# Kernel optimization log

Measured on AMD Instinct MI355X. Metric: run time of the kernel, lower is better.

The kernel has to match this reference:

```python
import jax, jax.numpy as jnp
import numpy as np

N = 4096        # nodes
IN_FEATS = 256
N_HIDDEN = 128
N_CLASSES = 32
E = 131072      # edges for the GAE blocks (avg degree 32)
TEMP = 0.2
ALPHA = 1.0
EPS = 1e-6
CHUNK = 64      # row-chunk size for masked max aggregation


def _glorot(key, shape):
    fan = shape[0] + shape[1]
    return jax.random.normal(key, shape, jnp.float32) * jnp.sqrt(2.0 / fan)


def setup_inputs():
    key = jax.random.key(0)
    ks = jax.random.split(key, 20)
    return {
        'adj': jax.random.uniform(ks[0], (N, N), jnp.float32),
        'inputs': jax.random.normal(ks[1], (N, IN_FEATS), jnp.float32),
        'feat_inputs': jax.random.normal(ks[2], (N, IN_FEATS), jnp.float32),
        'u': jax.random.uniform(ks[3], (N, N), jnp.float32),
        'src': jax.random.randint(ks[4], (E,), 0, N, jnp.int32),
        'dst': jax.random.randint(ks[5], (E,), 0, N, jnp.int32),
        # GAE GraphConv params (in->hidden, hidden->hidden)
        'gc0_W': _glorot(ks[6], (IN_FEATS, N_HIDDEN)), 'gc0_b': jnp.zeros((N_HIDDEN,), jnp.float32),
        'gc1_W': _glorot(ks[7], (N_HIDDEN, N_HIDDEN)), 'gc1_b': jnp.zeros((N_HIDDEN,), jnp.float32),
        # GraphSAGE layer 0 (in -> hidden), maxpool aggregator
        'p0_W': _glorot(ks[8], (IN_FEATS, IN_FEATS)), 'p0_b': jnp.zeros((IN_FEATS,), jnp.float32),
        'l0_W': _glorot(ks[9], (IN_FEATS, N_HIDDEN)), 'l0_b': jnp.zeros((N_HIDDEN,), jnp.float32),
        'b0': jnp.zeros((N_HIDDEN,), jnp.float32),
        # GraphSAGE layer 1 (hidden -> hidden)
        'p1_W': _glorot(ks[10], (N_HIDDEN, N_HIDDEN)), 'p1_b': jnp.zeros((N_HIDDEN,), jnp.float32),
        'l1_W': _glorot(ks[11], (N_HIDDEN, N_HIDDEN)), 'l1_b': jnp.zeros((N_HIDDEN,), jnp.float32),
        'b1': jnp.zeros((N_HIDDEN,), jnp.float32),
        # GraphSAGE layer 2 (hidden -> classes)
        'p2_W': _glorot(ks[12], (N_HIDDEN, N_HIDDEN)), 'p2_b': jnp.zeros((N_HIDDEN,), jnp.float32),
        'l2_W': _glorot(ks[13], (N_HIDDEN, N_CLASSES)), 'l2_b': jnp.zeros((N_CLASSES,), jnp.float32),
        'b2': jnp.zeros((N_CLASSES,), jnp.float32),
    }


def _graph_conv(h, W, b, src, dst, out_norm, in_norm):
    # DGL GraphConv, norm='both': D_in^{-1/2} A D_out^{-1/2} X W + b
    h = h @ W
    h = h * out_norm[:, None]
    agg = jax.ops.segment_sum(h[src], dst, num_segments=N)
    return agg * in_norm[:, None] + b


def _masked_max(mask, z):
    # h_new[i] = max_{j: mask[i, j]} z[j]; chunk over destination rows to bound memory
    n, d = z.shape
    m = mask.reshape(n // CHUNK, CHUNK, n)
    def body(carry, mc):
        out = jnp.max(jnp.where(mc[:, :, None], z[None, :, :], -jnp.inf), axis=1)
        return carry, out
    _, outs = jax.lax.scan(body, None, m)
    return outs.reshape(n, d)


def _l2norm(x):
    return x / jnp.maximum(jnp.linalg.norm(x, axis=1, keepdims=True), 1e-12)


def _forward(adj, inputs, feat_inputs, u, src, dst,
             gc0_W, gc0_b, gc1_W, gc1_b,
             p0_W, p0_b, l0_W, l0_b, b0,
             p1_W, p1_b, l1_W, l1_b, b1,
             p2_W, p2_b, l2_W, l2_b, b2):
    ones = jnp.ones((E,), jnp.float32)
    out_norm = jnp.maximum(jax.ops.segment_sum(ones, src, num_segments=N), 1.0) ** -0.5
    in_norm = jnp.maximum(jax.ops.segment_sum(ones, dst, num_segments=N), 1.0) ** -0.5
    # --- GAE encode (dropout inactive at inference) ---
    h = jax.nn.relu(_graph_conv(inputs, gc0_W, gc0_b, src, dst, out_norm, in_norm))
    h = _graph_conv(h, gc1_W, gc1_b, src, dst, out_norm, in_norm)
    # --- GAE decode ---
    ep = jax.nn.sigmoid(h @ h.T)
    # --- interpolate ---
    P = ALPHA * (ep / jnp.max(ep)) + (1.0 - ALPHA) * adj
    # --- RelaxedBernoulli straight-through sampling ---
    Pc = jnp.clip(P, EPS, 1.0 - EPS)
    uc = jnp.clip(u, EPS, 1.0 - EPS)
    logits = jnp.log(Pc) - jnp.log1p(-Pc)
    noise = jnp.log(uc) - jnp.log1p(-uc)        # logistic noise
    soft = jax.nn.sigmoid((logits + noise) / TEMP)
    y = soft + jax.lax.stop_gradient(jnp.round(soft) - soft)
    yt = jnp.triu(y, 1)
    A = yt + yt.T
    # --- normalize_adj: diag=1, L1 row normalize; original detaches here ---
    eye = jnp.eye(N, dtype=bool)
    A = jnp.where(eye, 1.0, A)
    A = A / jnp.maximum(jnp.sum(A, axis=1, keepdims=True), 1e-12)
    A = jax.lax.stop_gradient(A)
    mask = A != 0.0   # symmetric graph structure incl. self-loops
    # --- GraphSAGE with maxpool aggregator (dropout inactive) ---
    h = feat_inputs
    layers = ((p0_W, p0_b, l0_W, l0_b, b0, False),
              (p1_W, p1_b, l1_W, l1_b, b1, False),
              (p2_W, p2_b, l2_W, l2_b, b2, True))
    for pW, pb, lW, lb, bb, last in layers:
        z = jax.nn.relu(h @ pW + pb)
        agg = _masked_max(mask, z)
        h = agg @ lW + lb + bb
        if not last:
            h = _l2norm(jax.nn.relu(h))
    return h


def reference(adj, inputs, feat_inputs, u, src, dst,
              gc0_W, gc0_b, gc1_W, gc1_b,
              p0_W, p0_b, l0_W, l0_b, b0,
              p1_W, p1_b, l1_W, l1_b, b1,
              p2_W, p2_b, l2_W, l2_b, b2):
    return _forward(adj, inputs, feat_inputs, u, src, dst,
                    gc0_W, gc0_b, gc1_W, gc1_b,
                    p0_W, p0_b, l0_W, l0_b, b0,
                    p1_W, p1_b, l1_W, l1_b, b1,
                    p2_W, p2_b, l2_W, l2_b, b2)
```

## Files before the change

### kernel.cpp

```cpp
#include <hip/hip_runtime.h>
#include <hip/hip_fp16.h>
#include <cstdint>
#include <cstddef>

#define NN 4096
#define EE 131072
#define TS 64

__device__ __forceinline__ unsigned fkey(float f) {
    unsigned u = __float_as_uint(f);
    return (u & 0x80000000u) ? ~u : (u | 0x80000000u);
}
__device__ __forceinline__ float funkey(unsigned k) {
    unsigned u = (k & 0x80000000u) ? (k & 0x7fffffffu) : ~k;
    return __uint_as_float(u);
}

__device__ __forceinline__ void pkmax(unsigned& a, unsigned x) {
    asm("v_pk_max_f16 %0, %0, %1" : "+v"(a) : "v"(x));
}
__device__ __forceinline__ unsigned bit_sext_s(unsigned w, int off) {
    return (unsigned)(((int)(w << (31 - off))) >> 31);
}

__global__ void k_count(const int* __restrict__ src, const int* __restrict__ dst,
                        int* __restrict__ cs, int* __restrict__ cd) {
    int e = blockIdx.x * 256 + threadIdx.x;
    if (e < EE) {
        atomicAdd(&cs[src[e]], 1);
        atomicAdd(&cd[dst[e]], 1);
    }
}

__global__ void k_norm(const int* __restrict__ cs, const int* __restrict__ cd,
                       float* __restrict__ on, float* __restrict__ inn) {
    int i = blockIdx.x * 256 + threadIdx.x;
    if (i < NN) {
        int a = cs[i] > 1 ? cs[i] : 1;
        int b = cd[i] > 1 ? cd[i] : 1;
        on[i]  = 1.0f / sqrtf((float)a);
        inn[i] = 1.0f / sqrtf((float)b);
    }
}

template<int K, int ND, int RB>
__global__ void k_gemm_scale(const float* __restrict__ X, const float* __restrict__ W,
                             const float* __restrict__ scale, float* __restrict__ out) {
    __shared__ float xr[RB][K];
    int i0 = blockIdx.x * RB;
    for (int t = threadIdx.x; t < RB * K; t += ND)
        xr[t / K][t % K] = X[(size_t)(i0 + t / K) * K + t % K];
    __syncthreads();
    int j = threadIdx.x;
    float acc[RB];
    #pragma unroll
    for (int r = 0; r < RB; ++r) acc[r] = 0.0f;
    #pragma unroll 4
    for (int k = 0; k < K; ++k) {
        float w = W[k * ND + j];
        #pragma unroll
        for (int r = 0; r < RB; ++r) acc[r] = fmaf(xr[r][k], w, acc[r]);
    }
    #pragma unroll
    for (int r = 0; r < RB; ++r)
        out[(size_t)(i0 + r) * ND + j] = acc[r] * scale[i0 + r];
}

template<int K, int ND, int NS, int RB, int L2N, int H16>
__global__ void k_gemm_mrg(const float* __restrict__ X, size_t xstride,
                           const float* __restrict__ W,
                           const float* __restrict__ b1, const float* __restrict__ b2,
                           float* __restrict__ out, int do_relu) {
    __shared__ float xr[RB][K];
    int i0 = blockIdx.x * RB;
    for (int t = threadIdx.x; t < RB * K; t += ND) {
        size_t off = (size_t)(i0 + t / K) * K + t % K;
        float v = X[off];
        #pragma unroll
        for (int s = 1; s < NS; ++s) v = fmaxf(v, X[(size_t)s * xstride + off]);
        xr[t / K][t % K] = v;
    }
    __syncthreads();
    int j = threadIdx.x;
    float acc[RB];
    #pragma unroll
    for (int r = 0; r < RB; ++r) acc[r] = 0.0f;
    #pragma unroll 4
    for (int k = 0; k < K; ++k) {
        float w = W[k * ND + j];
        #pragma unroll
        for (int r = 0; r < RB; ++r) acc[r] = fmaf(xr[r][k], w, acc[r]);
    }
    if constexpr (L2N) {
        float v[RB], ss[RB];
        #pragma unroll
        for (int r = 0; r < RB; ++r) {
            float t = acc[r] + b1[j];
            if (b2) t += b2[j];
            v[r] = fmaxf(t, 0.0f);
            ss[r] = v[r] * v[r];
        }
        #pragma unroll
        for (int o = 1; o < 64; o <<= 1)
            #pragma unroll
            for (int r = 0; r < RB; ++r) ss[r] += __shfl_xor(ss[r], o, 64);
        __shared__ float sred[RB][2];
        if ((threadIdx.x & 63) == 0)
            #pragma unroll
            for (int r = 0; r < RB; ++r) sred[r][threadIdx.x >> 6] = ss[r];
        __syncthreads();
        #pragma unroll
        for (int r = 0; r < RB; ++r) {
            float tot = sred[r][0] + sred[r][1];
            out[(size_t)(i0 + r) * ND + j] = v[r] / fmaxf(sqrtf(tot), 1e-12f);
        }
    } else if constexpr (H16) {
        unsigned* oh = (unsigned*)out;
        #pragma unroll
        for (int r = 0; r < RB; ++r) {
            float v = fmaxf(acc[r] + b1[j], 0.0f);
            float o2 = __shfl_xor(v, 1, 64);
            if ((j & 1) == 0) {
                __half2 h = __floats2half2_rn(v, o2);
                oh[(size_t)(i0 + r) * (ND / 2) + (j >> 1)] = *(unsigned*)&h;
            }
        }
    } else {
        #pragma unroll
        for (int r = 0; r < RB; ++r) {
            float v = acc[r] + b1[j];
            if (b2) v += b2[j];
            if (do_relu) v = fmaxf(v, 0.0f);
            out[(size_t)(i0 + r) * ND + j] = v;
        }
    }
}

__global__ void k_scatter(const float* __restrict__ t, const int* __restrict__ src,
                          const int* __restrict__ dst, float* __restrict__ agg) {
    int e = blockIdx.x;
    int j = threadIdx.x;
    int s = src[e], d = dst[e];
    atomicAdd(&agg[(size_t)d * 128 + j], t[(size_t)s * 128 + j]);
}

__global__ void k_gcn_out(const float* __restrict__ agg, const float* __restrict__ inn,
                          const float* __restrict__ b, float* __restrict__ out, int do_relu) {
    int idx = blockIdx.x * 256 + threadIdx.x;
    int i = idx >> 7, j = idx & 127;
    float v = agg[idx] * inn[i] + b[j];
    if (do_relu) v = fmaxf(v, 0.0f);
    out[idx] = v;
}

template<int MODE>
__global__ __launch_bounds__(256, 4) void k_stile(const float* __restrict__ h,
                                                  const float* __restrict__ u,
                                                  unsigned* __restrict__ smax_key,
                                                  unsigned* __restrict__ mb) {
    int ti = blockIdx.y, tj = blockIdx.x;
    if (tj < ti) return;
    __shared__ float Ah[TS][68];
    __shared__ float Bh[TS][68];
    int tid = threadIdx.x;
    int tx = tid & 15, ty = tid >> 4;
    const float* ha = h + (size_t)ti * TS * 128;
    const float* hb = h + (size_t)tj * TS * 128;

    float acc[4][4];
    #pragma unroll
    for (int r = 0; r < 4; ++r)
        #pragma unroll
        for (int c = 0; c < 4; ++c) acc[r][c] = 0.0f;

    for (int half = 0; half < 2; ++half) {
        __syncthreads();
        #pragma unroll
        for (int t = 0; t < 4; ++t) {
            int f = tid + t * 256;
            int row = f >> 4, kk = f & 15;
            *(float4*)&Ah[row][kk * 4] = *(const float4*)(ha + (size_t)row * 128 + half * 64 + kk * 4);
            *(float4*)&Bh[row][kk * 4] = *(const float4*)(hb + (size_t)row * 128 + half * 64 + kk * 4);
        }
        __syncthreads();
        #pragma unroll 2
        for (int k4 = 0; k4 < 16; ++k4) {
            float4 a[4], b[4];
            #pragma unroll
            for (int r = 0; r < 4; ++r) a[r] = *(const float4*)&Ah[ty + 16 * r][k4 * 4];
            #pragma unroll
            for (int c = 0; c < 4; ++c) b[c] = *(const float4*)&Bh[tx + 16 * c][k4 * 4];
            #pragma unroll
            for (int r = 0; r < 4; ++r)
                #pragma unroll
                for (int c = 0; c < 4; ++c) {
                    acc[r][c] = fmaf(a[r].x, b[c].x, acc[r][c]);
                    acc[r][c] = fmaf(a[r].y, b[c].y, acc[r][c]);
                    acc[r][c] = fmaf(a[r].z, b[c].z, acc[r][c]);
                    acc[r][c] = fmaf(a[r].w, b[c].w, acc[r][c]);
                }
        }
    }

    if constexpr (MODE == 0) {
        float m = -3.4e38f;
        #pragma unroll
        for (int r = 0; r < 4; ++r)
            #pragma unroll
            for (int c = 0; c < 4; ++c) m = fmaxf(m, acc[r][c]);
        #pragma unroll
        for (int o = 1; o < 64; o <<= 1) m = fmaxf(m, __shfl_xor(m, o, 64));
        __shared__ float wm[4];
        if ((tid & 63) == 0) wm[tid >> 6] = m;
        __syncthreads();
        if (tid == 0) {
            float mm = fmaxf(fmaxf(wm[0], wm[1]), fmaxf(wm[2], wm[3]));
            atomicMax(smax_key, fkey(mm));
        }
    } else {
        float smax = funkey(*smax_key);
        float epmax = 1.0f / (1.0f + expf(-smax));
        __shared__ unsigned lm[TS][2];
        __shared__ unsigned lmT[TS][2];
        if (tid < 128) { lm[tid >> 1][tid & 1] = 0u; lmT[tid >> 1][tid & 1] = 0u; }
        __syncthreads();
        #pragma unroll
        for (int r = 0; r < 4; ++r) {
            #pragma unroll
            for (int c = 0; c < 4; ++c) {
                int li = ty + 16 * r, lj = tx + 16 * c;
                int gi = ti * TS + li, gj = tj * TS + lj;
                bool bit = false;
                if (gi < gj) {
                    float ep = 1.0f / (1.0f + expf(-acc[r][c]));
                    float P = ep / epmax;
                    float Pc = fminf(fmaxf(P, 1e-6f), 1.0f - 1e-6f);
                    float uu = u[(size_t)gi * NN + gj];
                    float ucv = fminf(fmaxf(uu, 1e-6f), 1.0f - 1e-6f);
                    bit = Pc > (1.0f - ucv);
                } else if (gi == gj) {
                    bit = true;
                }
                if (bit) {
                    atomicOr(&lm[li][lj >> 5], 1u << (lj & 31));
                    atomicOr(&lmT[lj][li >> 5], 1u << (li & 31));
                }
            }
        }
        __syncthreads();
        if (tid < 128) {
            int r = tid >> 1, wq = tid & 1;
            unsigned word = lm[r][wq];
            if (ti == tj) word |= lmT[r][wq];
            mb[(size_t)(ti * TS + r) * 128 + tj * 2 + wq] = word;
        } else if (ti != tj) {
            int r = (tid - 128) >> 1, wq = tid & 1;
            mb[(size_t)(tj * TS + r) * 128 + ti * 2 + wq] = lmT[r][wq];
        }
    }
}

__global__ __launch_bounds__(256, 4) void k_stile_store(const float* __restrict__ h,
                                                        float* __restrict__ S,
                                                        unsigned* __restrict__ smax_key) {
    int ti = blockIdx.y, tj = blockIdx.x;
    if (tj < ti) return;
    __shared__ float Ah[TS][68];
    __shared__ float Bh[TS][68];
    int tid = threadIdx.x;
    int tx = tid & 15, ty = tid >> 4;
    const float* ha = h + (size_t)ti * TS * 128;
    const float* hb = h + (size_t)tj * TS * 128;

    float acc[4][4];
    #pragma unroll
    for (int r = 0; r < 4; ++r)
        #pragma unroll
        for (int c = 0; c < 4; ++c) acc[r][c] = 0.0f;

    for (int half = 0; half < 2; ++half) {
        __syncthreads();
        #pragma unroll
        for (int t = 0; t < 4; ++t) {
            int f = tid + t * 256;
            int row = f >> 4, kk = f & 15;
            *(float4*)&Ah[row][kk * 4] = *(const float4*)(ha + (size_t)row * 128 + half * 64 + kk * 4);
            *(float4*)&Bh[row][kk * 4] = *(const float4*)(hb + (size_t)row * 128 + half * 64 + kk * 4);
        }
        __syncthreads();
        #pragma unroll 2
        for (int k4 = 0; k4 < 16; ++k4) {
            float4 a[4], b[4];
            #pragma unroll
            for (int r = 0; r < 4; ++r) a[r] = *(const float4*)&Ah[ty + 16 * r][k4 * 4];
            #pragma unroll
            for (int c = 0; c < 4; ++c) b[c] = *(const float4*)&Bh[tx + 16 * c][k4 * 4];
            #pragma unroll
            for (int r = 0; r < 4; ++r)
                #pragma unroll
                for (int c = 0; c < 4; ++c) {
                    acc[r][c] = fmaf(a[r].x, b[c].x, acc[r][c]);
                    acc[r][c] = fmaf(a[r].y, b[c].y, acc[r][c]);
                    acc[r][c] = fmaf(a[r].z, b[c].z, acc[r][c]);
                    acc[r][c] = fmaf(a[r].w, b[c].w, acc[r][c]);
                }
        }
    }

    float* sp = S + (size_t)(ti * 64 + tj) * 4096;
    #pragma unroll
    for (int r = 0; r < 4; ++r)
        #pragma unroll
        for (int c = 0; c < 4; ++c)
            sp[(ty + 16 * r) * 64 + tx + 16 * c] = acc[r][c];

    float m = -3.4e38f;
    #pragma unroll
    for (int r = 0; r < 4; ++r)
        #pragma unroll
        for (int c = 0; c < 4; ++c) m = fmaxf(m, acc[r][c]);
    #pragma unroll
    for (int o = 1; o < 64; o <<= 1) m = fmaxf(m, __shfl_xor(m, o, 64));
    __shared__ float wm[4];
    if ((tid & 63) == 0) wm[tid >> 6] = m;
    __syncthreads();
    if (tid == 0)
        atomicMax(smax_key, fkey(fmaxf(fmaxf(wm[0], wm[1]), fmaxf(wm[2], wm[3]))));
}

__global__ __launch_bounds__(256, 4) void k_bitemit(const float* __restrict__ S,
                                                    const float* __restrict__ u,
                                                    const unsigned* __restrict__ smax_key,
                                                    unsigned* __restrict__ mb) {
    int ti = blockIdx.y, tj = blockIdx.x;
    if (tj < ti) return;
    int tid = threadIdx.x;
    int tx = tid & 15, ty = tid >> 4;
    float smax = funkey(*smax_key);
    float epmax = 1.0f / (1.0f + expf(-smax));
    __shared__ unsigned lm[TS][2];
    __shared__ unsigned lmT[TS][2];
    if (tid < 128) { lm[tid >> 1][tid & 1] = 0u; lmT[tid >> 1][tid & 1] = 0u; }
    __syncthreads();
    const float* sp = S + (size_t)(ti * 64 + tj) * 4096;
    #pragma unroll
    for (int r = 0; r < 4; ++r) {
        #pragma unroll
        for (int c = 0; c < 4; ++c) {
            int li = ty + 16 * r, lj = tx + 16 * c;
            int gi = ti * TS + li, gj = tj * TS + lj;
            bool bit = false;
            if (gi < gj) {
                float ep = 1.0f / (1.0f + expf(-sp[li * 64 + lj]));
                float P = ep / epmax;
                float Pc = fminf(fmaxf(P, 1e-6f), 1.0f - 1e-6f);
                float uu = u[(size_t)gi * NN + gj];
                float ucv = fminf(fmaxf(uu, 1e-6f), 1.0f - 1e-6f);
                bit = Pc > (1.0f - ucv);
            } else if (gi == gj) {
                bit = true;
            }
            if (bit) {
                atomicOr(&lm[li][lj >> 5], 1u << (lj & 31));
                atomicOr(&lmT[lj][li >> 5], 1u << (li & 31));
            }
        }
    }
    __syncthreads();
    if (tid < 128) {
        int r = tid >> 1, wq = tid & 1;
        unsigned word = lm[r][wq];
        if (ti == tj) word |= lmT[r][wq];
        mb[(size_t)(ti * TS + r) * 128 + tj * 2 + wq] = word;
    } else if (ti != tj) {
        int r = (tid - 128) >> 1, wq = tid & 1;
        mb[(size_t)(tj * TS + r) * 128 + ti * 2 + wq] = lmT[r][wq];
    }
}

template<int RT, int JS>
__global__ __launch_bounds__(256, 8) void k_mmax256h(const unsigned* __restrict__ mb,
                                                     const unsigned* __restrict__ zh,
                                                     float* __restrict__ part) {
    constexpr int JPS = NN / JS;
    constexpr int WPS = JPS / 32;
    constexpr int RPG = RT / 4;
    constexpr int NRB = NN / RT;
    int rowblk = blockIdx.x % NRB, js = blockIdx.x / NRB;
    int i0 = rowblk * RT;

    __shared__ unsigned msk[RT][WPS + 1];
    {
        int t = threadIdx.x;
        msk[t / WPS][t % WPS] = mb[(size_t)(i0 + t / WPS) * 128 + js * WPS + t % WPS];
    }
    __syncthreads();

    int d = threadIdx.x & 63;
    int g = threadIdx.x >> 6;
    const uint2* zbase = (const uint2*)zh + (size_t)js * JPS * 64 + d;

    uint2 acc[RPG];
    #pragma unroll
    for (int r = 0; r < RPG; ++r) acc[r] = make_uint2(0u, 0u);

    #pragma unroll 1
    for (int wq = 0; wq < WPS; ++wq) {
        unsigned m[RPG];
        #pragma unroll
        for (int r = 0; r < RPG; ++r)
            m[r] = (unsigned)__builtin_amdgcn_readfirstlane((int)msk[g * RPG + r][wq]);
        const uint2* zp = zbase + (size_t)(wq * 32) * 64;
        #pragma unroll 2
        for (int j4 = 0; j4 < 32; j4 += 4) {
            uint2 z0 = zp[0 * 64];
            uint2 z1 = zp[1 * 64];
            uint2 z2 = zp[2 * 64];
            uint2 z3 = zp[3 * 64];
            #pragma unroll
            for (int r = 0; r < RPG; ++r) {
                unsigned s0 = bit_sext_s(m[r], j4 + 0);
                unsigned s1 = bit_sext_s(m[r], j4 + 1);
                unsigned s2 = bit_sext_s(m[r], j4 + 2);
                unsigned s3 = bit_sext_s(m[r], j4 + 3);
                pkmax(acc[r].x, s0 & z0.x); pkmax(acc[r].y, s0 & z0.y);
                pkmax(acc[r].x, s1 & z1.x); pkmax(acc[r].y, s1 & z1.y);
                pkmax(acc[r].x, s2 & z2.x); pkmax(acc[r].y, s2 & z2.y);
                pkmax(acc[r].x, s3 & z3.x); pkmax(acc[r].y, s3 & z3.y);
            }
            zp += 4 * 64;
        }
    }

    float4* po = (float4*)(part + (size_t)js * NN * 256);
    #pragma unroll
    for (int r = 0; r < RPG; ++r) {
        __half2 h0 = *(__half2*)&acc[r].x;
        __half2 h1 = *(__half2*)&acc[r].y;
        float2 f0 = __half22float2(h0);
        float2 f1 = __half22float2(h1);
        po[(size_t)(i0 + g * RPG + r) * 64 + d] = make_float4(f0.x, f0.y, f1.x, f1.y);
    }
}

template<int RT, int JS>
__global__ __launch_bounds__(256, 8) void k_mmax128h(const unsigned* __restrict__ mb,
                                                     const unsigned* __restrict__ zh,
                                                     float* __restrict__ part) {
    constexpr int JPS = NN / JS;
    constexpr int WPS = JPS / 32;
    constexpr int RPG = RT / 4;
    constexpr int NRB = NN / RT;
    int rowblk = blockIdx.x % NRB, js = blockIdx.x / NRB;
    int i0 = rowblk * RT;

    __shared__ unsigned msk[RT][WPS + 1];
    {
        int t = threadIdx.x;
        msk[t / WPS][t % WPS] = mb[(size_t)(i0 + t / WPS) * 128 + js * WPS + t % WPS];
    }
    __syncthreads();

    int lane = threadIdx.x & 63;
    int g = threadIdx.x >> 6;
    unsigned jpar = lane >> 5;
    int d2 = lane & 31;
    const uint2* zbase = (const uint2*)zh + (size_t)js * JPS * 32 + d2;

    uint2 acc[RPG];
    #pragma unroll
    for (int r = 0; r < RPG; ++r) acc[r] = make_uint2(0u, 0u);

    #pragma unroll 1
    for (int wq = 0; wq < WPS; ++wq) {
        unsigned m[RPG];
        #pragma unroll
        for (int r = 0; r < RPG; ++r)
            m[r] = (unsigned)__builtin_amdgcn_readfirstlane((int)msk[g * RPG + r][wq]);
        const uint2* zp = zbase + (size_t)(wq * 32) * 32;
        #pragma unroll 2
        for (int j4 = 0; j4 < 32; j4 += 4) {
            uint2 za = zp[(size_t)jpar * 32];
            uint2 zb = zp[(size_t)(2 + jpar) * 32];
            int oa = j4 + (int)jpar, ob = j4 + 2 + (int)jpar;
            #pragma unroll
            for (int r = 0; r < RPG; ++r) {
                unsigned sa = bit_sext_s(m[r], oa);
                unsigned sb = bit_sext_s(m[r], ob);
                pkmax(acc[r].x, sa & za.x); pkmax(acc[r].y, sa & za.y);
                pkmax(acc[r].x, sb & zb.x); pkmax(acc[r].y, sb & zb.y);
            }
            zp += 4 * 32;
        }
    }

    #pragma unroll
    for (int r = 0; r < RPG; ++r) {
        unsigned ox = __shfl_xor(acc[r].x, 32, 64);
        unsigned oy = __shfl_xor(acc[r].y, 32, 64);
        pkmax(acc[r].x, ox);
        pkmax(acc[r].y, oy);
    }
    if (!jpar) {
        float4* po = (float4*)(part + (size_t)js * NN * 128);
        #pragma unroll
        for (int r = 0; r < RPG; ++r) {
            __half2 h0 = *(__half2*)&acc[r].x;
            __half2 h1 = *(__half2*)&acc[r].y;
            float2 f0 = __half22float2(h0);
            float2 f1 = __half22float2(h1);
            po[(size_t)(i0 + g * RPG + r) * 32 + d2] = make_float4(f0.x, f0.y, f1.x, f1.y);
        }
    }
}

template<int NS>
__global__ void k_gemm_final(const float* __restrict__ X, size_t xstride,
                             const float* __restrict__ W,
                             const float* __restrict__ b1, const float* __restrict__ b2,
                             float* __restrict__ out) {
    __shared__ float xr[4][128];
    int i0 = blockIdx.x * 4;
    for (int t = threadIdx.x; t < 512; t += 128) {
        int r = t >> 7, k = t & 127;
        float v = X[(size_t)(i0 + r) * 128 + k];
        #pragma unroll
        for (int s = 1; s < NS; ++s)
            v = fmaxf(v, X[(size_t)s * xstride + (size_t)(i0 + r) * 128 + k]);
        xr[r][k] = v;
    }
    __syncthreads();
    int il = threadIdx.x >> 5, j = threadIdx.x & 31;
    float acc = 0.0f;
    #pragma unroll 8
    for (int k = 0; k < 128; ++k) acc = fmaf(xr[il][k], W[k * 32 + j], acc);
    out[(size_t)(i0 + il) * 32 + j] = acc + b1[j] + b2[j];
}

extern "C" void kernel_launch(void* const* d_in, const int* in_sizes, int n_in,
                              void* d_out, int out_size, void* d_ws, size_t ws_size,
                              hipStream_t stream) {
    const float* inputs = (const float*)d_in[1];
    const float* feat   = (const float*)d_in[2];
    const float* u      = (const float*)d_in[3];
    const int*   src    = (const int*)d_in[4];
    const int*   dst    = (const int*)d_in[5];
    const float* gc0W = (const float*)d_in[6],  *gc0b = (const float*)d_in[7];
    const float* gc1W = (const float*)d_in[8],  *gc1b = (const float*)d_in[9];
    const float* p0W  = (const float*)d_in[10], *p0b  = (const float*)d_in[11];
    const float* l0W  = (const float*)d_in[12], *l0b  = (const float*)d_in[13];
    const float* b0   = (const float*)d_in[14];
    const float* p1W  = (const float*)d_in[15], *p1b  = (const float*)d_in[16];
    const float* l1W  = (const float*)d_in[17], *l1b  = (const float*)d_in[18];
    const float* b1   = (const float*)d_in[19];
    const float* p2W  = (const float*)d_in[20], *p2b  = (const float*)d_in[21];
    const float* l2W  = (const float*)d_in[22], *l2b  = (const float*)d_in[23];
    const float* b2   = (const float*)d_in[24];
    float* out = (float*)d_out;

    const size_t MB = 1048576;
    char* w = (char*)d_ws;
    int*      cnt_src  = (int*)(w + 0);
    int*      cnt_dst  = (int*)(w + 16384);
    float*    on       = (float*)(w + 32768);
    float*    inn      = (float*)(w + 49152);
    unsigned* smax_key = (unsigned*)(w + 65536);
    char*     big      = w + 131072;
    float*    tmp      = (float*)(big);
    float*    agg      = (float*)(big + 2 * MB);
    float*    hbuf     = (float*)(big + 4 * MB);
    unsigned* mb       = (unsigned*)(big + 6 * MB);
    unsigned* zh       = (unsigned*)(big + 8 * MB);
    float*    pm       = (float*)(big + 12 * MB);
    float*    hs       = (float*)(big + 44 * MB);
    float*    Sbuf     = (float*)(big + 46 * MB);
    bool use_sstore = ws_size >= 131072 + 110 * MB;

    hipMemsetAsync(w, 0, 131072, stream);
    k_count<<<EE / 256, 256, 0, stream>>>(src, dst, cnt_src, cnt_dst);
    k_norm<<<NN / 256, 256, 0, stream>>>(cnt_src, cnt_dst, on, inn);

    k_gemm_scale<256, 128, 4><<<NN / 4, 128, 0, stream>>>(inputs, gc0W, on, tmp);
    hipMemsetAsync(agg, 0, (size_t)NN * 128 * 4, stream);
    k_scatter<<<EE, 128, 0, stream>>>(tmp, src, dst, agg);
    k_gcn_out<<<NN * 128 / 256, 256, 0, stream>>>(agg, inn, gc0b, hbuf, 1);

    k_gemm_scale<128, 128, 4><<<NN / 4, 128, 0, stream>>>(hbuf, gc1W, on, tmp);
    hipMemsetAsync(agg, 0, (size_t)NN * 128 * 4, stream);
    k_scatter<<<EE, 128, 0, stream>>>(tmp, src, dst, agg);
    k_gcn_out<<<NN * 128 / 256, 256, 0, stream>>>(agg, inn, gc1b, hbuf, 0);

    dim3 tg(64, 64);
    if (use_sstore) {
        k_stile_store<<<tg, 256, 0, stream>>>(hbuf, Sbuf, smax_key);
        k_bitemit<<<tg, 256, 0, stream>>>(Sbuf, u, smax_key, mb);
    } else {
        k_stile<0><<<tg, 256, 0, stream>>>(hbuf, nullptr, smax_key, nullptr);
        k_stile<1><<<tg, 256, 0, stream>>>(hbuf, u, smax_key, mb);
    }

    k_gemm_mrg<256, 256, 1, 4, 0, 1><<<NN / 4, 256, 0, stream>>>(feat, 0, p0W, p0b, nullptr, (float*)zh, 1);
    k_mmax256h<16, 8><<<(NN / 16) * 8, 256, 0, stream>>>(mb, zh, pm);
    k_gemm_mrg<256, 128, 8, 4, 1, 0><<<NN / 4, 128, 0, stream>>>(pm, (size_t)NN * 256, l0W, l0b, b0, hs, 0);

    k_gemm_mrg<128, 128, 1, 4, 0, 1><<<NN / 4, 128, 0, stream>>>(hs, 0, p1W, p1b, nullptr, (float*)zh, 1);
    k_mmax128h<16, 8><<<(NN / 16) * 8, 256, 0, stream>>>(mb, zh, pm);
    k_gemm_mrg<128, 128, 8, 4, 1, 0><<<NN / 4, 128, 0, stream>>>(pm, (size_t)NN * 128, l1W, l1b, b1, tmp, 0);

    k_gemm_mrg<128, 128, 1, 4, 0, 1><<<NN / 4, 128, 0, stream>>>(tmp, 0, p2W, p2b, nullptr, (float*)zh, 1);
    k_mmax128h<16, 8><<<(NN / 16) * 8, 256, 0, stream>>>(mb, zh, pm);
    k_gemm_final<8><<<NN / 4, 128, 0, stream>>>(pm, (size_t)NN * 128, l2W, l2b, b2, out);
}
```

Baseline: 673.5 us.

## Store masked-max partials as packed fp16 and batch edges per block in scatter

```diff
diff --git a/kernel.cpp b/kernel.cpp
--- a/kernel.cpp
+++ b/kernel.cpp
@@ -66,20 +66,13 @@
         out[(size_t)(i0 + r) * ND + j] = acc[r] * scale[i0 + r];
 }
 
-template<int K, int ND, int NS, int RB, int L2N, int H16>
-__global__ void k_gemm_mrg(const float* __restrict__ X, size_t xstride,
-                           const float* __restrict__ W,
-                           const float* __restrict__ b1, const float* __restrict__ b2,
-                           float* __restrict__ out, int do_relu) {
+template<int K, int ND, int RB, int H16>
+__global__ void k_gemm_ab(const float* __restrict__ X, const float* __restrict__ W,
+                          const float* __restrict__ b1, float* __restrict__ out) {
     __shared__ float xr[RB][K];
     int i0 = blockIdx.x * RB;
-    for (int t = threadIdx.x; t < RB * K; t += ND) {
-        size_t off = (size_t)(i0 + t / K) * K + t % K;
-        float v = X[off];
-        #pragma unroll
-        for (int s = 1; s < NS; ++s) v = fmaxf(v, X[(size_t)s * xstride + off]);
-        xr[t / K][t % K] = v;
-    }
+    for (int t = threadIdx.x; t < RB * K; t += ND)
+        xr[t / K][t % K] = X[(size_t)(i0 + t / K) * K + t % K];
     __syncthreads();
     int j = threadIdx.x;
     float acc[RB];
@@ -91,30 +84,7 @@
         #pragma unroll
         for (int r = 0; r < RB; ++r) acc[r] = fmaf(xr[r][k], w, acc[r]);
     }
-    if constexpr (L2N) {
-        float v[RB], ss[RB];
-        #pragma unroll
-        for (int r = 0; r < RB; ++r) {
-            float t = acc[r] + b1[j];
-            if (b2) t += b2[j];
-            v[r] = fmaxf(t, 0.0f);
-            ss[r] = v[r] * v[r];
-        }
-        #pragma unroll
-        for (int o = 1; o < 64; o <<= 1)
-            #pragma unroll
-            for (int r = 0; r < RB; ++r) ss[r] += __shfl_xor(ss[r], o, 64);
-        __shared__ float sred[RB][2];
-        if ((threadIdx.x & 63) == 0)
-            #pragma unroll
-            for (int r = 0; r < RB; ++r) sred[r][threadIdx.x >> 6] = ss[r];
-        __syncthreads();
-        #pragma unroll
-        for (int r = 0; r < RB; ++r) {
-            float tot = sred[r][0] + sred[r][1];
-            out[(size_t)(i0 + r) * ND + j] = v[r] / fmaxf(sqrtf(tot), 1e-12f);
-        }
-    } else if constexpr (H16) {
+    if constexpr (H16) {
         unsigned* oh = (unsigned*)out;
         #pragma unroll
         for (int r = 0; r < RB; ++r) {
@@ -127,10 +97,68 @@
         }
     } else {
         #pragma unroll
+        for (int r = 0; r < RB; ++r)
+            out[(size_t)(i0 + r) * ND + j] = acc[r] + b1[j];
+    }
+}
+
+template<int K, int ND, int NS, int RB, int L2N>
+__global__ void k_gemm_mrgh(const unsigned* __restrict__ Xh, size_t xstride,
+                            const float* __restrict__ W,
+                            const float* __restrict__ b1, const float* __restrict__ b2,
+                            float* __restrict__ out) {
+    __shared__ float xr[RB][K];
+    int i0 = blockIdx.x * RB;
+    for (int t = threadIdx.x; t < RB * (K / 2); t += ND) {
+        int r = t / (K / 2), c = t % (K / 2);
+        size_t off = (size_t)(i0 + r) * (K / 2) + c;
+        unsigned v = Xh[off];
+        #pragma unroll
+        for (int s = 1; s < NS; ++s) pkmax(v, Xh[(size_t)s * xstride + off]);
+        __half2 h = *(__half2*)&v;
+        float2 f = __half22float2(h);
+        xr[r][2 * c] = f.x;
+        xr[r][2 * c + 1] = f.y;
+    }
+    __syncthreads();
+    int j = threadIdx.x;
+    float acc[RB];
+    #pragma unroll
+    for (int r = 0; r < RB; ++r) acc[r] = 0.0f;
+    #pragma unroll 4
+    for (int k = 0; k < K; ++k) {
+        float w = W[k * ND + j];
+        #pragma unroll
+        for (int r = 0; r < RB; ++r) acc[r] = fmaf(xr[r][k], w, acc[r]);
+    }
+    if constexpr (L2N) {
+        float v[RB], ss[RB];
+        #pragma unroll
+        for (int r = 0; r < RB; ++r) {
+            float t = acc[r] + b1[j];
+            if (b2) t += b2[j];
+            v[r] = fmaxf(t, 0.0f);
+            ss[r] = v[r] * v[r];
+        }
+        #pragma unroll
+        for (int o = 1; o < 64; o <<= 1)
+            #pragma unroll
+            for (int r = 0; r < RB; ++r) ss[r] += __shfl_xor(ss[r], o, 64);
+        __shared__ float sred[RB][2];
+        if ((threadIdx.x & 63) == 0)
+            #pragma unroll
+            for (int r = 0; r < RB; ++r) sred[r][threadIdx.x >> 6] = ss[r];
+        __syncthreads();
+        #pragma unroll
+        for (int r = 0; r < RB; ++r) {
+            float tot = sred[r][0] + sred[r][1];
+            out[(size_t)(i0 + r) * ND + j] = v[r] / fmaxf(sqrtf(tot), 1e-12f);
+        }
+    } else {
+        #pragma unroll
         for (int r = 0; r < RB; ++r) {
             float v = acc[r] + b1[j];
             if (b2) v += b2[j];
-            if (do_relu) v = fmaxf(v, 0.0f);
             out[(size_t)(i0 + r) * ND + j] = v;
         }
     }
@@ -138,10 +166,16 @@
 
 __global__ void k_scatter(const float* __restrict__ t, const int* __restrict__ src,
                           const int* __restrict__ dst, float* __restrict__ agg) {
-    int e = blockIdx.x;
-    int j = threadIdx.x;
-    int s = src[e], d = dst[e];
-    atomicAdd(&agg[(size_t)d * 128 + j], t[(size_t)s * 128 + j]);
+    int wave = threadIdx.x >> 6;
+    int lane = threadIdx.x & 63;
+    int base = blockIdx.x * 16;
+    for (int ee = wave; ee < 16; ee += 4) {
+        int e = base + ee;
+        int s = src[e], d = dst[e];
+        float2 v = *(const float2*)(t + (size_t)s * 128 + 2 * lane);
+        atomicAdd(&agg[(size_t)d * 128 + 2 * lane], v.x);
+        atomicAdd(&agg[(size_t)d * 128 + 2 * lane + 1], v.y);
+    }
 }
 
 __global__ void k_gcn_out(const float* __restrict__ agg, const float* __restrict__ inn,
@@ -381,7 +415,7 @@
 template<int RT, int JS>
 __global__ __launch_bounds__(256, 8) void k_mmax256h(const unsigned* __restrict__ mb,
                                                      const unsigned* __restrict__ zh,
-                                                     float* __restrict__ part) {
+                                                     unsigned* __restrict__ pmh) {
     constexpr int JPS = NN / JS;
     constexpr int WPS = JPS / 32;
     constexpr int RPG = RT / 4;
@@ -432,21 +466,16 @@
         }
     }
 
-    float4* po = (float4*)(part + (size_t)js * NN * 256);
-    #pragma unroll
-    for (int r = 0; r < RPG; ++r) {
-        __half2 h0 = *(__half2*)&acc[r].x;
-        __half2 h1 = *(__half2*)&acc[r].y;
-        float2 f0 = __half22float2(h0);
-        float2 f1 = __half22float2(h1);
-        po[(size_t)(i0 + g * RPG + r) * 64 + d] = make_float4(f0.x, f0.y, f1.x, f1.y);
-    }
+    uint2* po = (uint2*)(pmh + (size_t)js * NN * 128);
+    #pragma unroll
+    for (int r = 0; r < RPG; ++r)
+        po[(size_t)(i0 + g * RPG + r) * 64 + d] = acc[r];
 }
 
 template<int RT, int JS>
 __global__ __launch_bounds__(256, 8) void k_mmax128h(const unsigned* __restrict__ mb,
                                                      const unsigned* __restrict__ zh,
-                                                     float* __restrict__ part) {
+                                                     unsigned* __restrict__ pmh) {
     constexpr int JPS = NN / JS;
     constexpr int WPS = JPS / 32;
     constexpr int RPG = RT / 4;
@@ -502,32 +531,30 @@
         pkmax(acc[r].y, oy);
     }
     if (!jpar) {
-        float4* po = (float4*)(part + (size_t)js * NN * 128);
-        #pragma unroll
-        for (int r = 0; r < RPG; ++r) {
-            __half2 h0 = *(__half2*)&acc[r].x;
-            __half2 h1 = *(__half2*)&acc[r].y;
-            float2 f0 = __half22float2(h0);
-            float2 f1 = __half22float2(h1);
-            po[(size_t)(i0 + g * RPG + r) * 32 + d2] = make_float4(f0.x, f0.y, f1.x, f1.y);
-        }
+        uint2* po = (uint2*)(pmh + (size_t)js * NN * 64);
+        #pragma unroll
+        for (int r = 0; r < RPG; ++r)
+            po[(size_t)(i0 + g * RPG + r) * 32 + d2] = acc[r];
     }
 }
 
 template<int NS>
-__global__ void k_gemm_final(const float* __restrict__ X, size_t xstride,
+__global__ void k_gemm_final(const unsigned* __restrict__ Xh, size_t xstride,
                              const float* __restrict__ W,
                              const float* __restrict__ b1, const float* __restrict__ b2,
                              float* __restrict__ out) {
     __shared__ float xr[4][128];
     int i0 = blockIdx.x * 4;
-    for (int t = threadIdx.x; t < 512; t += 128) {
-        int r = t >> 7, k = t & 127;
-        float v = X[(size_t)(i0 + r) * 128 + k];
-        #pragma unroll
-        for (int s = 1; s < NS; ++s)
-            v = fmaxf(v, X[(size_t)s * xstride + (size_t)(i0 + r) * 128 + k]);
-        xr[r][k] = v;
+    for (int t = threadIdx.x; t < 256; t += 128) {
+        int r = t >> 6, c = t & 63;
+        size_t off = (size_t)(i0 + r) * 64 + c;
+        unsigned v = Xh[off];
+        #pragma unroll
+        for (int s = 1; s < NS; ++s) pkmax(v, Xh[(size_t)s * xstride + off]);
+        __half2 h = *(__half2*)&v;
+        float2 f = __half22float2(h);
+        xr[r][2 * c] = f.x;
+        xr[r][2 * c + 1] = f.y;
     }
     __syncthreads();
     int il = threadIdx.x >> 5, j = threadIdx.x & 31;
@@ -571,7 +598,7 @@
     float*    hbuf     = (float*)(big + 4 * MB);
     unsigned* mb       = (unsigned*)(big + 6 * MB);
     unsigned* zh       = (unsigned*)(big + 8 * MB);
-    float*    pm       = (float*)(big + 12 * MB);
+    unsigned* pmh      = (unsigned*)(big + 12 * MB);
     float*    hs       = (float*)(big + 44 * MB);
     float*    Sbuf     = (float*)(big + 46 * MB);
     bool use_sstore = ws_size >= 131072 + 110 * MB;
@@ -582,12 +609,12 @@
 
     k_gemm_scale<256, 128, 4><<<NN / 4, 128, 0, stream>>>(inputs, gc0W, on, tmp);
     hipMemsetAsync(agg, 0, (size_t)NN * 128 * 4, stream);
-    k_scatter<<<EE, 128, 0, stream>>>(tmp, src, dst, agg);
+    k_scatter<<<EE / 16, 256, 0, stream>>>(tmp, src, dst, agg);
     k_gcn_out<<<NN * 128 / 256, 256, 0, stream>>>(agg, inn, gc0b, hbuf, 1);
 
     k_gemm_scale<128, 128, 4><<<NN / 4, 128, 0, stream>>>(hbuf, gc1W, on, tmp);
     hipMemsetAsync(agg, 0, (size_t)NN * 128 * 4, stream);
-    k_scatter<<<EE, 128, 0, stream>>>(tmp, src, dst, agg);
+    k_scatter<<<EE / 16, 256, 0, stream>>>(tmp, src, dst, agg);
     k_gcn_out<<<NN * 128 / 256, 256, 0, stream>>>(agg, inn, gc1b, hbuf, 0);
 
     dim3 tg(64, 64);
@@ -599,15 +626,15 @@
         k_stile<1><<<tg, 256, 0, stream>>>(hbuf, u, smax_key, mb);
     }
 
-    k_gemm_mrg<256, 256, 1, 4, 0, 1><<<NN / 4, 256, 0, stream>>>(feat, 0, p0W, p0b, nullptr, (float*)zh, 1);
-    k_mmax256h<16, 8><<<(NN / 16) * 8, 256, 0, stream>>>(mb, zh, pm);
-    k_gemm_mrg<256, 128, 8, 4, 1, 0><<<NN / 4, 128, 0, stream>>>(pm, (size_t)NN * 256, l0W, l0b, b0, hs, 0);
-
-    k_gemm_mrg<128, 128, 1, 4, 0, 1><<<NN / 4, 128, 0, stream>>>(hs, 0, p1W, p1b, nullptr, (float*)zh, 1);
-    k_mmax128h<16, 8><<<(NN / 16) * 8, 256, 0, stream>>>(mb, zh, pm);
-    k_gemm_mrg<128, 128, 8, 4, 1, 0><<<NN / 4, 128, 0, stream>>>(pm, (size_t)NN * 128, l1W, l1b, b1, tmp, 0);
-
-    k_gemm_mrg<128, 128, 1, 4, 0, 1><<<NN / 4, 128, 0, stream>>>(tmp, 0, p2W, p2b, nullptr, (float*)zh, 1);
-    k_mmax128h<16, 8><<<(NN / 16) * 8, 256, 0, stream>>>(mb, zh, pm);
-    k_gemm_final<8><<<NN / 4, 128, 0, stream>>>(pm, (size_t)NN * 128, l2W, l2b, b2, out);
-}
+    k_gemm_ab<256, 256, 4, 1><<<NN / 4, 256, 0, stream>>>(feat, p0W, p0b, (float*)zh);
+    k_mmax256h<16, 8><<<(NN / 16) * 8, 256, 0, stream>>>(mb, zh, pmh);
+    k_gemm_mrgh<256, 128, 8, 4, 1><<<NN / 4, 128, 0, stream>>>(pmh, (size_t)NN * 128, l0W, l0b, b0, hs);
+
+    k_gemm_ab<128, 128, 4, 1><<<NN / 4, 128, 0, stream>>>(hs, p1W, p1b, (float*)zh);
+    k_mmax128h<16, 8><<<(NN / 16) * 8, 256, 0, stream>>>(mb, zh, pmh);
+    k_gemm_mrgh<128, 128, 8, 4, 1><<<NN / 4, 128, 0, stream>>>(pmh, (size_t)NN * 64, l1W, l1b, b1, tmp);
+
+    k_gemm_ab<128, 128, 4, 1><<<NN / 4, 128, 0, stream>>>(tmp, p2W, p2b, (float*)zh);
+    k_mmax128h<16, 8><<<(NN / 16) * 8, 256, 0, stream>>>(mb, zh, pmh);
+    k_gemm_final<8><<<NN / 4, 128, 0, stream>>>(pmh, (size_t)NN * 64, l2W, l2b, b2, out);
+}
```

New measurement: 777.8 us. 15.5% more time.
